# Optimization experiments

Hardware: AMD Instinct MI355X
Metric: run time of the kernel (lower is better)

## Reference

```python
import jax, jax.numpy as jnp
import numpy as np

EPS = 1e-6

def _quat_mul(q1, q2):
    # Hamilton product, broadcasting over leading dims; last dim = 4 (w,x,y,z)
    w1, x1, y1, z1 = jnp.moveaxis(q1, -1, 0)
    w2, x2, y2, z2 = jnp.moveaxis(q2, -1, 0)
    return jnp.stack([
        w1*w2 - x1*x2 - y1*y2 - z1*z2,
        w1*x2 + x1*w2 + y1*z2 - z1*y2,
        w1*y2 - x1*z2 + y1*w2 + z1*x2,
        w1*z2 + x1*y2 - y1*x2 + z1*w2,
    ], axis=-1)

def _quat_log(q):
    # log(q) = arccos(clamp(w)) * v/||v||, zero when ||v|| < EPS
    w = q[..., 0]
    v = q[..., 1:]
    v_norm = jnp.linalg.norm(v, axis=-1)
    safe = v_norm >= EPS
    scale = jnp.arccos(jnp.clip(w, -1.0, 1.0)) / jnp.where(safe, v_norm, 1.0)
    return jnp.where(safe[..., None], scale[..., None] * v, jnp.zeros_like(v))

def _quat_exp(omega):
    # exp(omega) = [cos||w||, sin||w|| * w/||w||]; identity when ||w|| < EPS
    theta = jnp.linalg.norm(omega, axis=-1)
    safe = theta >= EPS
    w = jnp.cos(theta)
    xyz = (jnp.sin(theta) / jnp.where(safe, theta, 1.0))[..., None] * omega
    q = jnp.concatenate([w[..., None], xyz], axis=-1)
    ident = jnp.array([1.0, 0.0, 0.0, 0.0], dtype=omega.dtype)
    return jnp.where(safe[..., None], q, ident)

def setup_inputs() -> dict:
    key = jax.random.key(0)
    k1, k2, k3, k4 = jax.random.split(key, 4)
    B = 2097152
    HORIZON = 10
    def unit_quat(k):
        q = jax.random.normal(k, (B, 4), dtype=jnp.float32)
        return q / jnp.linalg.norm(q, axis=-1, keepdims=True)
    q_prev = unit_quat(k1)
    q_curr = unit_quat(k2)
    # xavier_uniform with gain=0.1 for w1 [16,8] and w2 [4,16]
    lim1 = 0.1 * np.sqrt(6.0 / (16 + 8))
    lim2 = 0.1 * np.sqrt(6.0 / (4 + 16))
    w1 = jax.random.uniform(k3, (16, 8), dtype=jnp.float32, minval=-lim1, maxval=lim1)
    w2 = jax.random.uniform(k4, (4, 16), dtype=jnp.float32, minval=-lim2, maxval=lim2)
    b1 = jnp.zeros((16,), dtype=jnp.float32)
    b2 = jnp.zeros((4,), dtype=jnp.float32)
    t_steps = jnp.linspace(0.1, 1.0, HORIZON, dtype=jnp.float32)
    return {"q_prev": q_prev, "q_curr": q_curr, "w1": w1, "b1": b1,
            "w2": w2, "b2": b2, "t_steps": t_steps}

def reference(q_prev, q_curr, w1, b1, w2, b2, t_steps):
    # MLP velocity correction: [B,8] -> tanh -> [B,4]
    velocity_input = jnp.concatenate([q_prev, q_curr], axis=-1)       # [B,8]
    h = jnp.tanh(velocity_input @ w1.T + b1)                          # [B,16]
    velocity_correction = h @ w2.T + b2                               # [B,4]

    # omega = 2 * log(q_curr * conj(q_prev))  -> [B,3]
    conj = jnp.array([1.0, -1.0, -1.0, -1.0], dtype=q_prev.dtype)
    delta_q = _quat_mul(q_curr, q_prev * conj)
    omega = 2.0 * _quat_log(delta_q)

    # Constant-angular-velocity extrapolation over the horizon
    ot = omega[:, None, :] * t_steps[None, :, None]                   # [B,H,3]
    q_delta = _quat_exp(ot)                                           # [B,H,4]
    q_pred = _quat_mul(q_delta, q_curr[:, None, :])                   # [B,H,4]
    q_pred = q_pred + velocity_correction[:, None, :] * t_steps[None, :, None] * 0.1
    norm = jnp.maximum(jnp.linalg.norm(q_pred, axis=-1, keepdims=True), 1e-12)
    return q_pred / norm                                              # [B,H,4]
```

## Files before the change

### kernel.cpp

```cpp
#include <hip/hip_runtime.h>
#include <math.h>

#define EPS_F 1e-6f
#define BLOCK 128
#define STRIDE_DW 44

__global__ __launch_bounds__(BLOCK) void traj_kernel(
    const float4* __restrict__ q_prev,
    const float4* __restrict__ q_curr,
    const float*  __restrict__ w1,
    const float*  __restrict__ b1,
    const float*  __restrict__ w2,
    const float*  __restrict__ b2,
    const float*  __restrict__ t_steps,
    float4*       __restrict__ out,
    int B)
{
    __shared__ float lds[BLOCK * STRIDE_DW];

    const int tid = threadIdx.x;
    int i = blockIdx.x * BLOCK + tid;
    if (i >= B) i = B - 1;

    const float4 qp = q_prev[i];
    const float4 qc = q_curr[i];

    float in8[8] = {qp.x, qp.y, qp.z, qp.w, qc.x, qc.y, qc.z, qc.w};

    float h[16];
#pragma unroll
    for (int j = 0; j < 16; ++j) {
        float acc = b1[j];
#pragma unroll
        for (int k = 0; k < 8; ++k) acc = fmaf(w1[j * 8 + k], in8[k], acc);
        float e = __expf(2.0f * acc);
        h[j] = 1.0f - 2.0f / (e + 1.0f);
    }

    float vc[4];
#pragma unroll
    for (int j = 0; j < 4; ++j) {
        float acc = b2[j];
#pragma unroll
        for (int k = 0; k < 16; ++k) acc = fmaf(w2[j * 16 + k], h[k], acc);
        vc[j] = acc;
    }

    float dw =  qc.x*qp.x + qc.y*qp.y + qc.z*qp.z + qc.w*qp.w;
    float dx = -qc.x*qp.y + qc.y*qp.x - qc.z*qp.w + qc.w*qp.z;
    float dy = -qc.x*qp.z + qc.y*qp.w + qc.z*qp.x - qc.w*qp.y;
    float dz = -qc.x*qp.w - qc.y*qp.z + qc.z*qp.y + qc.w*qp.x;

    float vn  = sqrtf(dx*dx + dy*dy + dz*dz);
    float wcl = fminf(fmaxf(dw, -1.0f), 1.0f);
    float ang = acosf(wcl);
    bool  safe = (vn >= EPS_F);
    float inv_vn = safe ? (1.0f / vn) : 0.0f;
    float ux = dx * inv_vn, uy = dy * inv_vn, uz = dz * inv_vn;
    float on = safe ? (2.0f * ang) : 0.0f;

#pragma unroll
    for (int st = 0; st < 10; ++st) {
        float t  = t_steps[st];
        float th = on * t;
        float s, c;
        __sincosf(th, &s, &c);
        float ax = s * ux, ay = s * uy, az = s * uz;

        float pw = c*qc.x - ax*qc.y - ay*qc.z - az*qc.w;
        float px = c*qc.y + ax*qc.x + ay*qc.w - az*qc.z;
        float py = c*qc.z - ax*qc.w + ay*qc.x + az*qc.y;
        float pz = c*qc.w + ax*qc.z - ay*qc.y + az*qc.x;

        float tf = t * 0.1f;
        pw = fmaf(vc[0], tf, pw);
        px = fmaf(vc[1], tf, px);
        py = fmaf(vc[2], tf, py);
        pz = fmaf(vc[3], tf, pz);

        float n2 = pw*pw + px*px + py*py + pz*pz;
        float r  = rsqrtf(fmaxf(n2, 1e-24f));

        *(float4*)&lds[tid * STRIDE_DW + st * 4] =
            make_float4(pw*r, px*r, py*r, pz*r);
    }

    __syncthreads();

    const size_t base_f4  = (size_t)blockIdx.x * (BLOCK * 10);
    const size_t total_f4 = (size_t)B * 10;
#pragma unroll
    for (int k = 0; k < 10; ++k) {
        int g = k * BLOCK + tid;
        int e = g / 10;
        int s = g - e * 10;
        float4 v = *(const float4*)&lds[e * STRIDE_DW + s * 4];
        size_t gi = base_f4 + (size_t)g;
        if (gi < total_f4) out[gi] = v;
    }
}

extern "C" void kernel_launch(void* const* d_in, const int* in_sizes, int n_in,
                              void* d_out, int out_size, void* d_ws, size_t ws_size,
                              hipStream_t stream) {
    const float4* q_prev  = (const float4*)d_in[0];
    const float4* q_curr  = (const float4*)d_in[1];
    const float*  w1      = (const float*)d_in[2];
    const float*  b1      = (const float*)d_in[3];
    const float*  w2      = (const float*)d_in[4];
    const float*  b2      = (const float*)d_in[5];
    const float*  t_steps = (const float*)d_in[6];
    float4*       out     = (float4*)d_out;

    int B = in_sizes[0] / 4;
    int grid = (B + BLOCK - 1) / BLOCK;
    traj_kernel<<<grid, BLOCK, 0, stream>>>(q_prev, q_curr, w1, b1, w2, b2,
                                            t_steps, out, B);
}
```

Measured before the change: 84.78 us.

## Use persistent grid-stride blocks with prefetch of next tile's inputs

Replaces the one-tile-per-block launch with a persistent grid capped at 2048 blocks, each looping over tiles. The next tile's q_prev/q_curr loads are issued before the current tile's output stores, and the prelude MLP is computed while those stores drain. This is meant to overlap global loads with compute and stores and to cut block launch overhead. The risks are lower occupancy and parallelism from the capped grid. A tail tile is silently dropped when B is not a multiple of BLOCK, which does not occur for the given B.

```diff
diff --git a/kernel.cpp b/kernel.cpp
--- a/kernel.cpp
+++ b/kernel.cpp
@@ -4,6 +4,55 @@
 #define EPS_F 1e-6f
 #define BLOCK 128
 #define STRIDE_DW 44
+
+struct Pre {
+    float vc0, vc1, vc2, vc3;
+    float ux, uy, uz, on;
+};
+
+__device__ __forceinline__ Pre prelude(const float4 qp, const float4 qc,
+                                       const float* __restrict__ w1,
+                                       const float* __restrict__ b1,
+                                       const float* __restrict__ w2,
+                                       const float* __restrict__ b2)
+{
+    float in8[8] = {qp.x, qp.y, qp.z, qp.w, qc.x, qc.y, qc.z, qc.w};
+
+    float h[16];
+#pragma unroll
+    for (int j = 0; j < 16; ++j) {
+        float acc = b1[j];
+#pragma unroll
+        for (int k = 0; k < 8; ++k) acc = fmaf(w1[j * 8 + k], in8[k], acc);
+        float e = __expf(2.0f * acc);
+        h[j] = 1.0f - 2.0f / (e + 1.0f);
+    }
+
+    Pre r;
+    float vc[4];
+#pragma unroll
+    for (int j = 0; j < 4; ++j) {
+        float acc = b2[j];
+#pragma unroll
+        for (int k = 0; k < 16; ++k) acc = fmaf(w2[j * 16 + k], h[k], acc);
+        vc[j] = acc;
+    }
+    r.vc0 = vc[0]; r.vc1 = vc[1]; r.vc2 = vc[2]; r.vc3 = vc[3];
+
+    float dw =  qc.x*qp.x + qc.y*qp.y + qc.z*qp.z + qc.w*qp.w;
+    float dx = -qc.x*qp.y + qc.y*qp.x - qc.z*qp.w + qc.w*qp.z;
+    float dy = -qc.x*qp.z + qc.y*qp.w + qc.z*qp.x - qc.w*qp.y;
+    float dz = -qc.x*qp.w - qc.y*qp.z + qc.z*qp.y + qc.w*qp.x;
+
+    float vn  = sqrtf(dx*dx + dy*dy + dz*dz);
+    float wcl = fminf(fmaxf(dw, -1.0f), 1.0f);
+    float ang = acosf(wcl);
+    bool  safe = (vn >= EPS_F);
+    float inv_vn = safe ? (1.0f / vn) : 0.0f;
+    r.ux = dx * inv_vn; r.uy = dy * inv_vn; r.uz = dz * inv_vn;
+    r.on = safe ? (2.0f * ang) : 0.0f;
+    return r;
+}
 
 __global__ __launch_bounds__(BLOCK) void traj_kernel(
     const float4* __restrict__ q_prev,
@@ -19,84 +68,75 @@
     __shared__ float lds[BLOCK * STRIDE_DW];
 
     const int tid = threadIdx.x;
-    int i = blockIdx.x * BLOCK + tid;
-    if (i >= B) i = B - 1;
+    const int ntiles = B / BLOCK;
 
-    const float4 qp = q_prev[i];
-    const float4 qc = q_curr[i];
+    float tt[10];
+#pragma unroll
+    for (int s = 0; s < 10; ++s) tt[s] = t_steps[s];
 
-    float in8[8] = {qp.x, qp.y, qp.z, qp.w, qc.x, qc.y, qc.z, qc.w};
+    int T = blockIdx.x;
+    if (T >= ntiles) return;
 
-    float h[16];
-#pragma unroll
-    for (int j = 0; j < 16; ++j) {
-        float acc = b1[j];
-#pragma unroll
-        for (int k = 0; k < 8; ++k) acc = fmaf(w1[j * 8 + k], in8[k], acc);
-        float e = __expf(2.0f * acc);
-        h[j] = 1.0f - 2.0f / (e + 1.0f);
-    }
+    float4 qc = q_curr[(size_t)T * BLOCK + tid];
+    {
+        float4 qp = q_prev[(size_t)T * BLOCK + tid];
+        Pre cur = prelude(qp, qc, w1, b1, w2, b2);
 
-    float vc[4];
-#pragma unroll
-    for (int j = 0; j < 4; ++j) {
-        float acc = b2[j];
-#pragma unroll
-        for (int k = 0; k < 16; ++k) acc = fmaf(w2[j * 16 + k], h[k], acc);
-        vc[j] = acc;
-    }
-
-    float dw =  qc.x*qp.x + qc.y*qp.y + qc.z*qp.z + qc.w*qp.w;
-    float dx = -qc.x*qp.y + qc.y*qp.x - qc.z*qp.w + qc.w*qp.z;
-    float dy = -qc.x*qp.z + qc.y*qp.w + qc.z*qp.x - qc.w*qp.y;
-    float dz = -qc.x*qp.w - qc.y*qp.z + qc.z*qp.y + qc.w*qp.x;
-
-    float vn  = sqrtf(dx*dx + dy*dy + dz*dz);
-    float wcl = fminf(fmaxf(dw, -1.0f), 1.0f);
-    float ang = acosf(wcl);
-    bool  safe = (vn >= EPS_F);
-    float inv_vn = safe ? (1.0f / vn) : 0.0f;
-    float ux = dx * inv_vn, uy = dy * inv_vn, uz = dz * inv_vn;
-    float on = safe ? (2.0f * ang) : 0.0f;
+        while (true) {
+            const int Tn = T + gridDim.x;
+            const bool have_next = (Tn < ntiles);
 
 #pragma unroll
-    for (int st = 0; st < 10; ++st) {
-        float t  = t_steps[st];
-        float th = on * t;
-        float s, c;
-        __sincosf(th, &s, &c);
-        float ax = s * ux, ay = s * uy, az = s * uz;
+            for (int st = 0; st < 10; ++st) {
+                float t  = tt[st];
+                float th = cur.on * t;
+                float s, c;
+                __sincosf(th, &s, &c);
+                float ax = s * cur.ux, ay = s * cur.uy, az = s * cur.uz;
 
-        float pw = c*qc.x - ax*qc.y - ay*qc.z - az*qc.w;
-        float px = c*qc.y + ax*qc.x + ay*qc.w - az*qc.z;
-        float py = c*qc.z - ax*qc.w + ay*qc.x + az*qc.y;
-        float pz = c*qc.w + ax*qc.z - ay*qc.y + az*qc.x;
+                float pw = c*qc.x - ax*qc.y - ay*qc.z - az*qc.w;
+                float px = c*qc.y + ax*qc.x + ay*qc.w - az*qc.z;
+                float py = c*qc.z - ax*qc.w + ay*qc.x + az*qc.y;
+                float pz = c*qc.w + ax*qc.z - ay*qc.y + az*qc.x;
 
-        float tf = t * 0.1f;
-        pw = fmaf(vc[0], tf, pw);
-        px = fmaf(vc[1], tf, px);
-        py = fmaf(vc[2], tf, py);
-        pz = fmaf(vc[3], tf, pz);
+                float tf = t * 0.1f;
+                pw = fmaf(cur.vc0, tf, pw);
+                px = fmaf(cur.vc1, tf, px);
+                py = fmaf(cur.vc2, tf, py);
+                pz = fmaf(cur.vc3, tf, pz);
 
-        float n2 = pw*pw + px*px + py*py + pz*pz;
-        float r  = rsqrtf(fmaxf(n2, 1e-24f));
+                float n2 = pw*pw + px*px + py*py + pz*pz;
+                float r  = rsqrtf(fmaxf(n2, 1e-24f));
 
-        *(float4*)&lds[tid * STRIDE_DW + st * 4] =
-            make_float4(pw*r, px*r, py*r, pz*r);
-    }
+                *(float4*)&lds[tid * STRIDE_DW + st * 4] =
+                    make_float4(pw*r, px*r, py*r, pz*r);
+            }
 
-    __syncthreads();
+            __syncthreads();
 
-    const size_t base_f4  = (size_t)blockIdx.x * (BLOCK * 10);
-    const size_t total_f4 = (size_t)B * 10;
+            float4 qpn, qcn;
+            if (have_next) {
+                qpn = q_prev[(size_t)Tn * BLOCK + tid];
+                qcn = q_curr[(size_t)Tn * BLOCK + tid];
+            }
+
+            const size_t base = (size_t)T * (BLOCK * 10);
 #pragma unroll
-    for (int k = 0; k < 10; ++k) {
-        int g = k * BLOCK + tid;
-        int e = g / 10;
-        int s = g - e * 10;
-        float4 v = *(const float4*)&lds[e * STRIDE_DW + s * 4];
-        size_t gi = base_f4 + (size_t)g;
-        if (gi < total_f4) out[gi] = v;
+            for (int k = 0; k < 10; ++k) {
+                int g = k * BLOCK + tid;
+                int e = g / 10;
+                int s = g - e * 10;
+                out[base + g] = *(const float4*)&lds[e * STRIDE_DW + s * 4];
+            }
+
+            if (!have_next) break;
+
+            qc  = qcn;
+            cur = prelude(qpn, qcn, w1, b1, w2, b2);
+
+            __syncthreads();
+            T = Tn;
+        }
     }
 }
 
@@ -113,7 +153,8 @@
     float4*       out     = (float4*)d_out;
 
     int B = in_sizes[0] / 4;
-    int grid = (B + BLOCK - 1) / BLOCK;
+    int ntiles = (B + BLOCK - 1) / BLOCK;
+    int grid = ntiles < 2048 ? ntiles : 2048;
     traj_kernel<<<grid, BLOCK, 0, stream>>>(q_prev, q_curr, w1, b1, w2, b2,
                                             t_steps, out, B);
 }
```

After: 103.0 us. 1.21x slower.
